# Optimization experiments

Measured on AMD Instinct MI355X. Metric: run time of the kernel, lower is better.

Reference implementation:

```python
import jax, jax.numpy as jnp
import numpy as np

# config constants (from init_kwargs)
DT = 1.0
TAU_J = 10.0
TAU_M = 20.0
KAPPA_J = 0.25
A_GEN = 1.0
A_DISC = 1.0
THRESH = 0.4
X_DECAY = 20.0  # trace decay constant: x += -x/20 + spikes

B = 8192
LS = [1024, 512, 512, 256]


def setup_inputs() -> dict:
    key = jax.random.key(0)
    ks = jax.random.split(key, 24)
    inp = {}
    inp['x_input'] = (jax.random.uniform(ks[0], (B, LS[0])) < 0.2).astype(jnp.float32)
    inp['y_target'] = (jax.random.uniform(ks[1], (B, LS[3])) < 0.2).astype(jnp.float32)
    # hidden-layer states (layers 1 and 2); layer 0 / last are clamped
    inp['j1'] = jax.random.normal(ks[2], (B, LS[1])) * 0.1
    inp['v1'] = jax.random.normal(ks[3], (B, LS[1])) * 0.1
    inp['s1'] = (jax.random.uniform(ks[4], (B, LS[1])) < 0.2).astype(jnp.float32)
    inp['x1'] = jax.random.uniform(ks[5], (B, LS[1])) * 2.0
    inp['j2'] = jax.random.normal(ks[6], (B, LS[2])) * 0.1
    inp['v2'] = jax.random.normal(ks[7], (B, LS[2])) * 0.1
    inp['s2'] = (jax.random.uniform(ks[8], (B, LS[2])) < 0.2).astype(jnp.float32)
    inp['x2'] = jax.random.uniform(ks[9], (B, LS[2])) * 2.0
    # weights (torch.rand * 0.01)
    inp['W0'] = jax.random.uniform(ks[10], (LS[0], LS[1])) * 0.01
    inp['W1'] = jax.random.uniform(ks[11], (LS[1], LS[2])) * 0.01
    inp['W2'] = jax.random.uniform(ks[12], (LS[2], LS[3])) * 0.01
    inp['V0'] = jax.random.uniform(ks[13], (LS[1], LS[0])) * 0.01
    inp['V1'] = jax.random.uniform(ks[14], (LS[2], LS[1])) * 0.01
    inp['V2'] = jax.random.uniform(ks[15], (LS[3], LS[2])) * 0.01
    inp['Eg0'] = jax.random.uniform(ks[16], (LS[1], LS[0])) * 0.01
    inp['Eg1'] = jax.random.uniform(ks[17], (LS[2], LS[1])) * 0.01
    inp['Eg2'] = jax.random.uniform(ks[18], (LS[3], LS[2])) * 0.01
    inp['Ed0'] = jax.random.uniform(ks[19], (LS[0], LS[1])) * 0.01
    inp['Ed1'] = jax.random.uniform(ks[20], (LS[1], LS[2])) * 0.01
    inp['Ed2'] = jax.random.uniform(ks[21], (LS[2], LS[3])) * 0.01
    return inp


def _lif_update(j, v, x, total_input):
    # Eq 19-24: leaky current integrator -> leaky membrane -> threshold -> reset -> trace
    j = j + (DT / TAU_J) * (-KAPPA_J * j + total_input)
    v = v + (DT / TAU_M) * (-v + j)  # uses updated j, as in the torch code
    spikes = (v > THRESH).astype(v.dtype)
    v = v * (1.0 - spikes)  # hard reset
    x = x + (-x / X_DECAY + spikes)  # spike trace
    return j, v, spikes, x


def reference(x_input, y_target, j1, v1, s1, x1, j2, v2, s2, x2,
              W0, W1, W2, V0, V1, V2, Eg0, Eg1, Eg2, Ed0, Ed1, Ed2):
    # --- phase 1: error neurons (all layers, using current spikes) ---
    # layer 0 clamped: x0 = x_input, s0 = x_input; layer 3 clamped: x3 = s3 = y_target
    e_gen0 = A_GEN * (x_input - s1 @ W0.T)       # [B, 1024]
    e_gen1 = A_GEN * (x1 - s2 @ W1.T)            # [B, 512]
    e_gen2 = A_GEN * (x2 - y_target @ W2.T)      # [B, 512]
    e_disc1 = A_DISC * (x1 - x_input @ V0.T)     # [B, 512]
    e_disc2 = A_DISC * (x2 - s1 @ V1.T)          # [B, 512]
    e_disc3 = A_DISC * (y_target - s2 @ V2.T)    # [B, 256]

    # --- phase 2: value-neuron updates (hidden layers 1 and 2 only) ---
    total1 = -(e_gen1 + e_disc1) + e_gen0 @ Eg0.T + e_disc2 @ Ed1.T
    total2 = -(e_gen2 + e_disc2) + e_gen1 @ Eg1.T + e_disc3 @ Ed2.T

    j1n, v1n, s1n, x1n = _lif_update(j1, v1, x1, total1)
    j2n, v2n, s2n, x2n = _lif_update(j2, v2, x2, total2)

    return jnp.concatenate([j1n, v1n, x1n, s1n, j2n, v2n, x2n, s2n], axis=-1)  # [B, 4096]
```

## Files before the change

### kernel.cpp

```cpp
#include <hip/hip_runtime.h>
#include <stdint.h>
#include <stddef.h>

typedef unsigned short u16;
typedef __attribute__((ext_vector_type(8))) short short8;
typedef __attribute__((ext_vector_type(4))) float f32x4;

#define DEVI __device__ __forceinline__

DEVI u16 f2bf(float f) {
  union { float f; unsigned u; } c; c.f = f;
  unsigned r = c.u + 0x7fff + ((c.u >> 16) & 1);
  return (u16)(r >> 16);
}

DEVI short8 pack8(f32x4 a, f32x4 b) {
  short8 v;
#pragma unroll
  for (int i = 0; i < 4; i++) { v[i] = (short)f2bf(a[i]); v[i + 4] = (short)f2bf(b[i]); }
  return v;
}

typedef __attribute__((address_space(1))) const void global_cvoid;
typedef __attribute__((address_space(3))) void lds_void;


DEVI void mfma_phase(const u16* As, const u16* Bs, f32x4 acc[4][4])
{
  const int lane = threadIdx.x & 63;
  const int w    = threadIdx.x >> 6;
  const int l16  = lane & 15, lq = lane >> 4;
  const int wm   = (w >> 1) * 64, wn = (w & 1) * 64;
#pragma unroll
  for (int kc = 0; kc < 2; kc++) {
    short8 afr[4], bfr[4];
#pragma unroll
    for (int rt = 0; rt < 4; rt++) {
      int m  = wm + rt * 16 + l16;
      int gr = (kc * 4 + lq) ^ (m & 7);
      afr[rt] = *(const short8*)(As + m * 64 + gr * 8);
    }
#pragma unroll
    for (int ct = 0; ct < 4; ct++) {
      int n  = wn + ct * 16 + l16;
      int gr = (kc * 4 + lq) ^ (n & 7);
      bfr[ct] = *(const short8*)(Bs + n * 64 + gr * 8);
    }
#pragma unroll
    for (int rt = 0; rt < 4; rt++)
#pragma unroll
      for (int ct = 0; ct < 4; ct++)
        acc[rt][ct] = __builtin_amdgcn_mfma_f32_16x16x32_bf16(afr[rt], bfr[ct], acc[rt][ct], 0, 0, 0);
  }
}

DEVI void mfma_phase64(const u16* As, const u16* Bs, f32x4 acc[2][4])
{
  const int lane = threadIdx.x & 63;
  const int w    = threadIdx.x >> 6;
  const int l16  = lane & 15, lq = lane >> 4;
  const int wm   = (w >> 1) * 32, wn = (w & 1) * 64;
#pragma unroll
  for (int kc = 0; kc < 2; kc++) {
    short8 afr[2], bfr[4];
#pragma unroll
    for (int rt = 0; rt < 2; rt++) {
      int m  = wm + rt * 16 + l16;
      int gr = (kc * 4 + lq) ^ (m & 7);
      afr[rt] = *(const short8*)(As + m * 64 + gr * 8);
    }
#pragma unroll
    for (int ct = 0; ct < 4; ct++) {
      int n  = wn + ct * 16 + l16;
      int gr = (kc * 4 + lq) ^ (n & 7);
      bfr[ct] = *(const short8*)(Bs + n * 64 + gr * 8);
    }
#pragma unroll
    for (int rt = 0; rt < 2; rt++)
#pragma unroll
      for (int ct = 0; ct < 4; ct++)
        acc[rt][ct] = __builtin_amdgcn_mfma_f32_16x16x32_bf16(afr[rt], bfr[ct], acc[rt][ct], 0, 0, 0);
  }
}

DEVI void zero_acc(f32x4 acc[4][4]) {
  f32x4 z = {0.f, 0.f, 0.f, 0.f};
#pragma unroll
  for (int a = 0; a < 4; a++)
#pragma unroll
    for (int b = 0; b < 4; b++) acc[a][b] = z;
}

DEVI void zero_acc24(f32x4 acc[2][4]) {
  f32x4 z = {0.f, 0.f, 0.f, 0.f};
#pragma unroll
  for (int a = 0; a < 2; a++)
#pragma unroll
    for (int b = 0; b < 4; b++) acc[a][b] = z;
}

struct Params {
  const float *x_input, *y_target, *j1, *v1, *s1, *x1, *j2, *v2, *s2, *x2;
  const float *W0, *W1, *W2, *V0, *V1, *V2, *Eg0, *Eg1, *Ed1, *Ed2;
};


template <int RR>
DEVI void stage_async(const u16* gbase, int ldr, int k0, u16* lds)
{
  const int t = threadIdx.x;
  const int lane = t & 63, w = t >> 6;
#pragma unroll
  for (int tt = 0; tt < RR; tt++) {
    int rowbase = w * (RR * 8) + tt * 8;
    int row = rowbase + (lane >> 3);
    int gsw = (lane & 7) ^ (row & 7);
    __builtin_amdgcn_global_load_lds(
        (global_cvoid*)(gbase + (size_t)row * ldr + k0 + gsw * 8),
        (lds_void*)(lds + rowbase * 64), 16, 0, 0);
  }
}

DEVI void gemm_term_fast(const u16* A, const u16* B, int K,
                         u16* As, u16* Bs, f32x4 acc[4][4])
{
  for (int k0 = 0; k0 < K; k0 += 64) {
    stage_async<4>(A, K, k0, As);
    stage_async<4>(B, K, k0, Bs);
    __syncthreads();
    mfma_phase(As, Bs, acc);
    __syncthreads();
  }
}

DEVI void gemm_term_pipe(const u16* A, const u16* B, int K,
                         u16* As0, u16* As1, u16* Bs0, u16* Bs1, f32x4 acc[2][4])
{
  const int nt = K >> 6;
  stage_async<2>(A, K, 0, As0);
  stage_async<4>(B, K, 0, Bs0);
  stage_async<2>(A, K, 64, As1);
  stage_async<4>(B, K, 64, Bs1);
  for (int t = 0; t < nt; t++) {
    if (t < nt - 1) asm volatile("s_waitcnt vmcnt(6)" ::: "memory");
    else            asm volatile("s_waitcnt vmcnt(0)" ::: "memory");
    __builtin_amdgcn_s_barrier();
    __builtin_amdgcn_sched_barrier(0);
    if (t & 1) mfma_phase64(As1, Bs1, acc);
    else       mfma_phase64(As0, Bs0, acc);
    asm volatile("s_waitcnt lgkmcnt(0)" ::: "memory");
    __builtin_amdgcn_sched_barrier(0);
    __builtin_amdgcn_s_barrier();
    if (t + 2 < nt) {
      if (t & 1) { stage_async<2>(A, K, (t + 2) * 64, As1); stage_async<4>(B, K, (t + 2) * 64, Bs1); }
      else       { stage_async<2>(A, K, (t + 2) * 64, As0); stage_async<4>(B, K, (t + 2) * 64, Bs0); }
    }
  }
}

struct PJob { const float *s0, *s1; u16* dst; int start; };
struct TJob { const float* in; u16* out; int J, tbase; };
struct PrepArgs { PJob jb[14]; TJob tj[4]; };

__global__ __launch_bounds__(256) void k_prep(PrepArgs A)
{
  __shared__ u16 T[32][33];
  int b = blockIdx.x;
  int t = threadIdx.x;
  if (b < 14464) {
    int ji = 0;
#pragma unroll
    for (int i = 1; i < 14; i++)
      if (b >= A.jb[i].start) ji = i;
    PJob pj = A.jb[ji];
    size_t e0 = ((size_t)(b - pj.start) * 256 + t) * 8;
    const float* s0 = pj.s0 + e0;
    f32x4 a  = *(const f32x4*)s0;
    f32x4 b4 = *(const f32x4*)(s0 + 4);
    if (pj.s1) {
      const float* s1 = pj.s1 + e0;
      a  = a  + *(const f32x4*)s1;
      b4 = b4 + *(const f32x4*)(s1 + 4);
    }
    *(short8*)(pj.dst + e0) = pack8(a, b4);
    return;
  }
  int b2 = b - 14464;
  int ji = 0;
#pragma unroll
  for (int i = 1; i < 4; i++)
    if (b2 >= A.tj[i].tbase) ji = i;
  TJob jb = A.tj[ji];
  int local = b2 - jb.tbase;
  int tm = local >> 4;
  int tk = local & 15;
  int tx = t & 31, ty = t >> 5;
#pragma unroll
  for (int i = 0; i < 4; i++) {
    int r = ty + i * 8;
    T[r][tx] = f2bf(jb.in[(size_t)(tm * 32 + r) * 512 + tk * 32 + tx]);
  }
  __syncthreads();
#pragma unroll
  for (int i = 0; i < 4; i++) {
    int r = ty + i * 8;
    jb.out[(size_t)(tk * 32 + r) * jb.J + tm * 32 + tx] = T[tx][r];
  }
}

struct BW2Args {
  const u16 *Eg0b, *W0tb, *Ed1b, *V1tb, *Eg1b, *W1tb, *Ed2b, *V2tb;
  u16 *Bw1b, *Bw2b;
};

__global__ __launch_bounds__(256) void k_bw2(BW2Args A)
{
  __shared__ u16 As[128 * 64];
  __shared__ u16 Bs[128 * 64];
  int b   = blockIdx.x;
  int mat = b >> 4, loc = b & 15;
  int bmw = loc >> 2, bnw = loc & 3;

  f32x4 acc[4][4];
  zero_acc(acc);
  u16* dst;
  if (mat == 0) {
    gemm_term_fast(A.Eg0b + (size_t)bmw * 128 * 1024, A.W0tb + (size_t)bnw * 128 * 1024, 1024, As, Bs, acc);
    gemm_term_fast(A.Ed1b + (size_t)bmw * 128 * 512,  A.V1tb + (size_t)bnw * 128 * 512,   512, As, Bs, acc);
    dst = A.Bw1b;
  } else {
    gemm_term_fast(A.Eg1b + (size_t)bmw * 128 * 512,  A.W1tb + (size_t)bnw * 128 * 512,   512, As, Bs, acc);
    gemm_term_fast(A.Ed2b + (size_t)bmw * 128 * 256,  A.V2tb + (size_t)bnw * 128 * 256,   256, As, Bs, acc);
    dst = A.Bw2b;
  }
  const int lane = threadIdx.x & 63;
  const int w    = threadIdx.x >> 6;
  const int l16  = lane & 15, lq = lane >> 4;
  const int wm   = (w >> 1) * 64, wn = (w & 1) * 64;
#pragma unroll
  for (int rt = 0; rt < 4; rt++)
#pragma unroll
    for (int ct = 0; ct < 4; ct++)
#pragma unroll
      for (int i = 0; i < 4; i++) {
        int rl = wm + rt * 16 + lq * 4 + i;
        int cl = wn + ct * 16 + l16;
        dst[(size_t)(bmw * 128 + rl) * 512 + bnw * 128 + cl] = f2bf(-acc[rt][ct][i]);
      }
}

struct MJobF {
  const u16* A[4]; const u16* B[4]; int K[4];
  const float *jin, *vin, *xin;
  int obase;
};
struct MArgsF { MJobF j[2]; };

__global__ __launch_bounds__(256, 3) void k_main_fast(MArgsF P, float* __restrict__ out)
{
  __shared__ __align__(16) u16 As0[64 * 64];
  __shared__ __align__(16) u16 As1[64 * 64];
  __shared__ __align__(16) u16 Bs0[128 * 64];
  __shared__ __align__(16) u16 Bs1[128 * 64];
  int job   = blockIdx.x >> 9;
  int local = blockIdx.x & 511;
  int bm = local & 127, bn = local >> 7;
  MJobF jb = P.j[job];

  f32x4 acc[2][4];
  zero_acc24(acc);
#pragma unroll
  for (int p = 0; p < 4; p++)
    gemm_term_pipe(jb.A[p] + (size_t)bm * 64 * jb.K[p],
                   jb.B[p] + (size_t)bn * 128 * jb.K[p], jb.K[p],
                   As0, As1, Bs0, Bs1, acc);

  const int lane = threadIdx.x & 63;
  const int w    = threadIdx.x >> 6;
  const int l16  = lane & 15, lq = lane >> 4;
  const int wm   = (w >> 1) * 32, wn = (w & 1) * 64;

#pragma unroll
  for (int rt = 0; rt < 2; rt++)
#pragma unroll
    for (int ct = 0; ct < 4; ct++)
#pragma unroll
      for (int i = 0; i < 4; i++) {
        int row    = bm * 64 + wm + rt * 16 + lq * 4 + i;
        int col    = bn * 128 + wn + ct * 16 + l16;
        size_t idx = (size_t)row * 512 + col;
        float xf = jb.xin[idx];
        float total = acc[rt][ct][i] - 2.0f * xf;
        float jf = jb.jin[idx];
        float vf = jb.vin[idx];
        jf = jf + 0.1f * (-0.25f * jf + total);
        vf = vf + 0.05f * (-vf + jf);
        float sf = (vf > 0.4f) ? 1.0f : 0.0f;
        vf = vf * (1.0f - sf);
        xf = xf + (-xf / 20.0f + sf);
        size_t ob = (size_t)row * 4096 + jb.obase + col;
        out[ob]        = jf;
        out[ob + 512]  = vf;
        out[ob + 1024] = xf;
        out[ob + 1536] = sf;
      }
}


DEVI void stage_A_fb(const float* A, int ldr, int k0, u16* dst)
{
  const int t = threadIdx.x;
  const int g = t & 7, rb = t >> 3;
#pragma unroll
  for (int p = 0; p < 4; p++) {
    int row = p * 32 + rb;
    const float* src = A + (size_t)row * ldr + k0 + g * 8;
    f32x4 a = *(const f32x4*)src;
    f32x4 b = *(const f32x4*)(src + 4);
    *(short8*)(dst + row * 64 + (g ^ (row & 7)) * 8) = pack8(a, b);
  }
}

DEVI void nn_term_fb(const float* A, const float* B, int K, u16* As, u16* Bs, f32x4 acc[4][4])
{
  const int t  = threadIdx.x;
  const int ks = t >> 4, ng = t & 15;
  for (int k0 = 0; k0 < K; k0 += 64) {
    stage_A_fb(A, K, k0, As);
#pragma unroll
    for (int i = 0; i < 4; i++) {
      int kloc = i * 16 + ks;
      const float* src = B + (size_t)(k0 + kloc) * 512 + ng * 8;
      f32x4 a = *(const f32x4*)src;
      f32x4 b = *(const f32x4*)(src + 4);
#pragma unroll
      for (int e = 0; e < 8; e++) {
        int nloc = ng * 8 + e;
        float val = (e < 4) ? a[e] : b[e - 4];
        Bs[nloc * 64 + ((kloc >> 3) ^ (nloc & 7)) * 8 + (kloc & 7)] = f2bf(val);
      }
    }
    __syncthreads();
    mfma_phase(As, Bs, acc);
    __syncthreads();
  }
}

template <int MODE>
DEVI void gemm_term_fb(const float* A, const float* B0, const float* B1, int K,
                       u16* As, u16* Bs, f32x4 acc[4][4])
{
  const int t = threadIdx.x;
  const int g = t & 7, rb = t >> 3;
  for (int k0 = 0; k0 < K; k0 += 64) {
    stage_A_fb(A, K, k0, As);
#pragma unroll
    for (int p = 0; p < 4; p++) {
      int row = p * 32 + rb;
      const float* src;
      if (MODE == 2) src = B0 + (size_t)row * 4096 + (k0 >> 7) * 512 + (k0 & 127) + g * 8;
      else           src = B0 + (size_t)row * K + k0 + g * 8;
      f32x4 a = *(const f32x4*)src;
      f32x4 b = *(const f32x4*)(src + 4);
      if (MODE == 1) {
        const float* s2 = B1 + (size_t)row * K + k0 + g * 8;
        a = a + *(const f32x4*)s2;
        b = b + *(const f32x4*)(s2 + 4);
      }
      *(short8*)(Bs + row * 64 + (g ^ (row & 7)) * 8) = pack8(a, b);
    }
    __syncthreads();
    mfma_phase(As, Bs, acc);
    __syncthreads();
  }
}

__global__ __launch_bounds__(256) void k_bw_fb(Params P, float* __restrict__ out)
{
  __shared__ u16 As[128 * 64];
  __shared__ u16 Bs[128 * 64];
  int b   = blockIdx.x;
  int mat = b >> 4, loc = b & 15;
  int bmw = loc >> 2, bnw = loc & 3;

  f32x4 acc[4][4];
  zero_acc(acc);
  int obase;
  if (mat == 0) {
    nn_term_fb(P.Eg0 + (size_t)bmw * 128 * 1024, P.W0 + bnw * 128, 1024, As, Bs, acc);
    nn_term_fb(P.Ed1 + (size_t)bmw * 128 * 512,  P.V1 + bnw * 128,  512, As, Bs, acc);
    obase = 0;
  } else {
    nn_term_fb(P.Eg1 + (size_t)bmw * 128 * 512,  P.W1 + bnw * 128,  512, As, Bs, acc);
    nn_term_fb(P.Ed2 + (size_t)bmw * 128 * 256,  P.V2 + bnw * 128,  256, As, Bs, acc);
    obase = 2048;
  }
  const int lane = threadIdx.x & 63;
  const int w    = threadIdx.x >> 6;
  const int l16  = lane & 15, lq = lane >> 4;
  const int wm   = (w >> 1) * 64, wn = (w & 1) * 64;
#pragma unroll
  for (int rt = 0; rt < 4; rt++)
#pragma unroll
    for (int ct = 0; ct < 4; ct++)
#pragma unroll
      for (int i = 0; i < 4; i++) {
        int rl = wm + rt * 16 + lq * 4 + i;
        int cl = wn + ct * 16 + l16;
        out[(size_t)rl * 4096 + obase + bmw * 128 + bnw * 512 + cl] = -acc[rt][ct][i];
      }
}

__global__ __launch_bounds__(256) void k_main_fb(Params P, float* __restrict__ out, int fix)
{
  __shared__ u16 As[128 * 64];
  __shared__ u16 Bs[128 * 64];
  int job, bm, bn;
  if (fix) {
    job = blockIdx.x >> 2; bn = blockIdx.x & 3; bm = 0;
  } else {
    job = blockIdx.x >> 8;
    int local = blockIdx.x & 255;
    bm = local & 63; bn = local >> 6;
    if (bm == 0) return;
  }

  f32x4 acc[4][4];
  zero_acc(acc);
  const float *jin, *vin, *xin;
  int obase;
  size_t am = (size_t)bm * 128;

  if (job == 0) {
    gemm_term_fb<0>(P.s2      + am * 512,  P.W1  + (size_t)bn * 128 * 512,  nullptr, 512,  As, Bs, acc);
    gemm_term_fb<1>(P.x_input + am * 1024, P.V0  + (size_t)bn * 128 * 1024,
                    P.Eg0 + (size_t)bn * 128 * 1024, 1024, As, Bs, acc);
    gemm_term_fb<0>(P.x2      + am * 512,  P.Ed1 + (size_t)bn * 128 * 512,  nullptr, 512,  As, Bs, acc);
    gemm_term_fb<2>(P.s1      + am * 512,  out + 0 + bn * 128,              nullptr, 512,  As, Bs, acc);
    jin = P.j1; vin = P.v1; xin = P.x1; obase = 0;
  } else {
    gemm_term_fb<1>(P.y_target + am * 256, P.W2  + (size_t)bn * 128 * 256,
                    P.Ed2 + (size_t)bn * 128 * 256, 256, As, Bs, acc);
    gemm_term_fb<0>(P.s1      + am * 512,  P.V1  + (size_t)bn * 128 * 512,  nullptr, 512,  As, Bs, acc);
    gemm_term_fb<0>(P.x1      + am * 512,  P.Eg1 + (size_t)bn * 128 * 512,  nullptr, 512,  As, Bs, acc);
    gemm_term_fb<2>(P.s2      + am * 512,  out + 2048 + bn * 128,           nullptr, 512,  As, Bs, acc);
    jin = P.j2; vin = P.v2; xin = P.x2; obase = 2048;
  }

  const int lane = threadIdx.x & 63;
  const int w    = threadIdx.x >> 6;
  const int l16  = lane & 15, lq = lane >> 4;
  const int wm   = (w >> 1) * 64, wn = (w & 1) * 64;

#pragma unroll
  for (int rt = 0; rt < 4; rt++)
#pragma unroll
    for (int ct = 0; ct < 4; ct++)
#pragma unroll
      for (int i = 0; i < 4; i++) {
        int row    = bm * 128 + wm + rt * 16 + lq * 4 + i;
        int col    = bn * 128 + wn + ct * 16 + l16;
        size_t idx = (size_t)row * 512 + col;
        float xf = xin[idx];
        float total = acc[rt][ct][i] - 2.0f * xf;
        float jf = jin[idx];
        float vf = vin[idx];
        jf = jf + 0.1f * (-0.25f * jf + total);
        vf = vf + 0.05f * (-vf + jf);
        float sf = (vf > 0.4f) ? 1.0f : 0.0f;
        vf = vf * (1.0f - sf);
        xf = xf + (-xf / 20.0f + sf);
        size_t ob = (size_t)row * 4096 + obase + col;
        out[ob]        = jf;
        out[ob + 512]  = vf;
        out[ob + 1024] = xf;
        out[ob + 1536] = sf;
      }
}

extern "C" void kernel_launch(void* const* d_in, const int* in_sizes, int n_in,
                              void* d_out, int out_size, void* d_ws, size_t ws_size,
                              hipStream_t stream)
{
  Params P;
  P.x_input  = (const float*)d_in[0];
  P.y_target = (const float*)d_in[1];
  P.j1 = (const float*)d_in[2];
  P.v1 = (const float*)d_in[3];
  P.s1 = (const float*)d_in[4];
  P.x1 = (const float*)d_in[5];
  P.j2 = (const float*)d_in[6];
  P.v2 = (const float*)d_in[7];
  P.s2 = (const float*)d_in[8];
  P.x2 = (const float*)d_in[9];
  P.W0 = (const float*)d_in[10];
  P.W1 = (const float*)d_in[11];
  P.W2 = (const float*)d_in[12];
  P.V0 = (const float*)d_in[13];
  P.V1 = (const float*)d_in[14];
  P.V2 = (const float*)d_in[15];
  P.Eg0 = (const float*)d_in[16];
  P.Eg1 = (const float*)d_in[17];
  P.Ed1 = (const float*)d_in[20];
  P.Ed2 = (const float*)d_in[21];
  (void)in_sizes; (void)n_in; (void)out_size;

  float* out = (float*)d_out;

  if (ws_size >= 62652416) {
    char* ws = (char*)d_ws;
    u16* xin_b = (u16*)(ws + 0);
    u16* y_b   = (u16*)(ws + 16777216);
    u16* s1_b  = (u16*)(ws + 20971520);
    u16* x1_b  = (u16*)(ws + 29360128);
    u16* s2_b  = (u16*)(ws + 37748736);
    u16* x2_b  = (u16*)(ws + 46137344);
    u16* W1_b  = (u16*)(ws + 54525952);
    u16* P1_b  = (u16*)(ws + 55050240);
    u16* Ed1_b = (u16*)(ws + 56098816);
    u16* V1_b  = (u16*)(ws + 56623104);
    u16* Eg1_b = (u16*)(ws + 57147392);
    u16* P2_b  = (u16*)(ws + 57671680);
    u16* Bw1_b = (u16*)(ws + 57933824);
    u16* Bw2_b = (u16*)(ws + 58458112);
    u16* W0t_b = (u16*)(ws + 58982400);
    u16* V1t_b = (u16*)(ws + 60030976);
    u16* W1t_b = (u16*)(ws + 60555264);
    u16* V2t_b = (u16*)(ws + 61079552);
    u16* Eg0_b = (u16*)(ws + 61341696);
    u16* Ed2_b = (u16*)(ws + 62390272);

    PrepArgs pa;
    pa.jb[0]  = { P.x_input,  nullptr, xin_b,     0 };
    pa.jb[1]  = { P.y_target, nullptr, y_b,    4096 };
    pa.jb[2]  = { P.s1,       nullptr, s1_b,   5120 };
    pa.jb[3]  = { P.x1,       nullptr, x1_b,   7168 };
    pa.jb[4]  = { P.s2,       nullptr, s2_b,   9216 };
    pa.jb[5]  = { P.x2,       nullptr, x2_b,  11264 };
    pa.jb[6]  = { P.W1,       nullptr, W1_b,  13312 };
    pa.jb[7]  = { P.V0,       P.Eg0,   P1_b,  13440 };
    pa.jb[8]  = { P.Ed1,      nullptr, Ed1_b, 13696 };
    pa.jb[9]  = { P.V1,       nullptr, V1_b,  13824 };
    pa.jb[10] = { P.Eg1,      nullptr, Eg1_b, 13952 };
    pa.jb[11] = { P.W2,       P.Ed2,   P2_b,  14080 };
    pa.jb[12] = { P.Eg0,      nullptr, Eg0_b, 14144 };
    pa.jb[13] = { P.Ed2,      nullptr, Ed2_b, 14400 };
    pa.tj[0]  = { P.W0, W0t_b, 1024,    0 };
    pa.tj[1]  = { P.V1, V1t_b,  512,  512 };
    pa.tj[2]  = { P.W1, W1t_b,  512,  768 };
    pa.tj[3]  = { P.V2, V2t_b,  256, 1024 };
    k_prep<<<dim3(15616), dim3(256), 0, stream>>>(pa);

    BW2Args ba;
    ba.Eg0b = Eg0_b; ba.W0tb = W0t_b; ba.Ed1b = Ed1_b; ba.V1tb = V1t_b;
    ba.Eg1b = Eg1_b; ba.W1tb = W1t_b; ba.Ed2b = Ed2_b; ba.V2tb = V2t_b;
    ba.Bw1b = Bw1_b; ba.Bw2b = Bw2_b;
    k_bw2<<<dim3(32), dim3(256), 0, stream>>>(ba);

    MArgsF ma;
    ma.j[0].A[0] = s2_b;  ma.j[0].B[0] = W1_b;  ma.j[0].K[0] = 512;
    ma.j[0].A[1] = xin_b; ma.j[0].B[1] = P1_b;  ma.j[0].K[1] = 1024;
    ma.j[0].A[2] = x2_b;  ma.j[0].B[2] = Ed1_b; ma.j[0].K[2] = 512;
    ma.j[0].A[3] = s1_b;  ma.j[0].B[3] = Bw1_b; ma.j[0].K[3] = 512;
    ma.j[0].jin = P.j1; ma.j[0].vin = P.v1; ma.j[0].xin = P.x1; ma.j[0].obase = 0;
    ma.j[1].A[0] = y_b;   ma.j[1].B[0] = P2_b;  ma.j[1].K[0] = 256;
    ma.j[1].A[1] = s1_b;  ma.j[1].B[1] = V1_b;  ma.j[1].K[1] = 512;
    ma.j[1].A[2] = x1_b;  ma.j[1].B[2] = Eg1_b; ma.j[1].K[2] = 512;
    ma.j[1].A[3] = s2_b;  ma.j[1].B[3] = Bw2_b; ma.j[1].K[3] = 512;
    ma.j[1].jin = P.j2; ma.j[1].vin = P.v2; ma.j[1].xin = P.x2; ma.j[1].obase = 2048;
    k_main_fast<<<dim3(1024), dim3(256), 0, stream>>>(ma, out);
  } else {
    k_bw_fb<<<dim3(32), dim3(256), 0, stream>>>(P, out);
    k_main_fb<<<dim3(512), dim3(256), 0, stream>>>(P, out, 0);
    k_main_fb<<<dim3(8), dim3(256), 0, stream>>>(P, out, 1);
  }
}
```

Measured before the change: 433.0 us.

## Replace double-buffered pipeline with single-buffer loop, higher occupancy, staggered block starts

Drops the explicit double-buffered async-copy pipeline in the main fused GEMM kernel and goes back to a simple single-buffer load/sync/compute loop. Halving the shared memory lets launch bounds rise from 3 to 4 blocks per CU. Blocks also get a staggered start through s_sleep delays that depend on block index, so they fall out of phase and their loads overlap other blocks' compute. The trade is losing in-block prefetch overlap in return for more resident blocks and desynchronized memory traffic.

Result: faster. 407.4 us (-5.9%).

```diff
diff --git a/kernel.cpp b/kernel.cpp
--- a/kernel.cpp
+++ b/kernel.cpp
@@ -133,28 +133,15 @@
   }
 }
 
-DEVI void gemm_term_pipe(const u16* A, const u16* B, int K,
-                         u16* As0, u16* As1, u16* Bs0, u16* Bs1, f32x4 acc[2][4])
-{
-  const int nt = K >> 6;
-  stage_async<2>(A, K, 0, As0);
-  stage_async<4>(B, K, 0, Bs0);
-  stage_async<2>(A, K, 64, As1);
-  stage_async<4>(B, K, 64, Bs1);
-  for (int t = 0; t < nt; t++) {
-    if (t < nt - 1) asm volatile("s_waitcnt vmcnt(6)" ::: "memory");
-    else            asm volatile("s_waitcnt vmcnt(0)" ::: "memory");
-    __builtin_amdgcn_s_barrier();
-    __builtin_amdgcn_sched_barrier(0);
-    if (t & 1) mfma_phase64(As1, Bs1, acc);
-    else       mfma_phase64(As0, Bs0, acc);
-    asm volatile("s_waitcnt lgkmcnt(0)" ::: "memory");
-    __builtin_amdgcn_sched_barrier(0);
-    __builtin_amdgcn_s_barrier();
-    if (t + 2 < nt) {
-      if (t & 1) { stage_async<2>(A, K, (t + 2) * 64, As1); stage_async<4>(B, K, (t + 2) * 64, Bs1); }
-      else       { stage_async<2>(A, K, (t + 2) * 64, As0); stage_async<4>(B, K, (t + 2) * 64, Bs0); }
-    }
+DEVI void gemm_term_main(const u16* A, const u16* B, int K,
+                         u16* As, u16* Bs, f32x4 acc[2][4])
+{
+  for (int k0 = 0; k0 < K; k0 += 64) {
+    stage_async<2>(A, K, k0, As);
+    stage_async<4>(B, K, k0, Bs);
+    __syncthreads();
+    mfma_phase64(As, Bs, acc);
+    __syncthreads();
   }
 }
 
@@ -256,24 +243,30 @@
 };
 struct MArgsF { MJobF j[2]; };
 
-__global__ __launch_bounds__(256, 3) void k_main_fast(MArgsF P, float* __restrict__ out)
-{
-  __shared__ __align__(16) u16 As0[64 * 64];
-  __shared__ __align__(16) u16 As1[64 * 64];
-  __shared__ __align__(16) u16 Bs0[128 * 64];
-  __shared__ __align__(16) u16 Bs1[128 * 64];
-  int job   = blockIdx.x >> 9;
-  int local = blockIdx.x & 511;
+__global__ __launch_bounds__(256, 4) void k_main_fast(MArgsF P, float* __restrict__ out)
+{
+  __shared__ u16 As[64 * 64];
+  __shared__ u16 Bs[128 * 64];
+  int bid   = blockIdx.x;
+  int job   = bid >> 9;
+  int local = bid & 511;
   int bm = local & 127, bn = local >> 7;
   MJobF jb = P.j[job];
 
+  switch (((bid >> 8) ^ bid) & 3) {
+    case 1: __builtin_amdgcn_s_sleep(8); break;
+    case 2: __builtin_amdgcn_s_sleep(8); __builtin_amdgcn_s_sleep(8); break;
+    case 3: __builtin_amdgcn_s_sleep(8); __builtin_amdgcn_s_sleep(8);
+            __builtin_amdgcn_s_sleep(8); break;
+    default: break;
+  }
+
   f32x4 acc[2][4];
   zero_acc24(acc);
 #pragma unroll
   for (int p = 0; p < 4; p++)
-    gemm_term_pipe(jb.A[p] + (size_t)bm * 64 * jb.K[p],
-                   jb.B[p] + (size_t)bn * 128 * jb.K[p], jb.K[p],
-                   As0, As1, Bs0, Bs1, acc);
+    gemm_term_main(jb.A[p] + (size_t)bm * 64 * jb.K[p],
+                   jb.B[p] + (size_t)bn * 128 * jb.K[p], jb.K[p], As, Bs, acc);
 
   const int lane = threadIdx.x & 63;
   const int w    = threadIdx.x >> 6;
```
